# Kernel optimization log

Measured on AMD Instinct MI355X. Metric: run time of the kernel, lower is better.

The kernel has to match this reference:

```python
import jax, jax.numpy as jnp
import numpy as np

XMIN, XMAX = -16.0, 16.0
ZMIN, ZMAX = -16.0, 16.0
SOFTCLIP_L = 5.0


def ref2mem(traj, Zs, Xs):
    # traj: (B, T, 2) cam (x, z) -> mem pixel coords
    x = (traj[..., 0] - XMIN) / ((XMAX - XMIN) / Xs) - 0.5
    z = (traj[..., 1] - ZMIN) / ((ZMAX - ZMIN) / Zs) - 0.5
    return x, z


def bilinear_sample2d(pm, x, z):
    # pm: (B, C, Z, X); x, z: (B, N) float coords -> (B, C, N)
    B, C, Zs, Xs = pm.shape
    x = jnp.clip(x, 0.0, Xs - 1.0)
    z = jnp.clip(z, 0.0, Zs - 1.0)
    x0 = jnp.floor(x).astype(jnp.int32)
    z0 = jnp.floor(z).astype(jnp.int32)
    x1 = jnp.minimum(x0 + 1, Xs - 1)
    z1 = jnp.minimum(z0 + 1, Zs - 1)
    wx = x - x0.astype(x.dtype)
    wz = z - z0.astype(z.dtype)
    pm_flat = pm.reshape(B, C, Zs * Xs)

    def gather(zi, xi):
        idx = (zi * Xs + xi)[:, None, :]  # (B,1,N)
        return jnp.take_along_axis(pm_flat, jnp.broadcast_to(idx, (B, C, idx.shape[-1])), axis=2)

    v00 = gather(z0, x0); v01 = gather(z0, x1)
    v10 = gather(z1, x0); v11 = gather(z1, x1)
    wx = wx[:, None, :]; wz = wz[:, None, :]
    return (v00 * (1 - wx) * (1 - wz) + v01 * wx * (1 - wz)
            + v10 * (1 - wx) * wz + v11 * wx * wz)


def gru_cell(x, h, W_ih, W_hh, b_ih, b_hh):
    gi = x @ W_ih.T + b_ih
    gh = h @ W_hh.T + b_hh
    i_r, i_z, i_n = jnp.split(gi, 3, axis=1)
    h_r, h_z, h_n = jnp.split(gh, 3, axis=1)
    r = jax.nn.sigmoid(i_r + h_r)
    z = jax.nn.sigmoid(i_z + h_z)
    n = jnp.tanh(i_n + r * h_n)
    return (1.0 - z) * n + z * h


def expm_softclip(sig_raw):
    B = sig_raw.shape[0]
    nrm = jnp.linalg.norm(sig_raw.reshape(B, -1), axis=1)
    denom = jax.nn.logsumexp(jnp.stack([nrm / SOFTCLIP_L, jnp.ones_like(nrm)], axis=-1), axis=-1)
    return sig_raw / denom[:, None, None]


def reference(feat_map, pred_map, noise, traj_past,
              W_ih, W_hh, b_ih, b_hh, past_W, past_b,
              W1, b1, W2, b2, W3, b3):
    B, C, Zf, Xf = feat_map.shape
    Zp, Xp = pred_map.shape[2], pred_map.shape[3]
    T_futu = noise.shape[1]
    H = W_hh.shape[1]
    eye2 = jnp.eye(2, dtype=feat_map.dtype)

    # static feature: max_pool2d k=8 s=8 + past encoding
    pooled = feat_map.reshape(B, C, Zf // 8, 8, Xf // 8, 8).max(axis=(3, 5)).reshape(B, -1)
    past_enc = traj_past.reshape(B, -1) @ past_W.T + past_b
    sta_feat = jnp.concatenate([pooled, past_enc], axis=1)  # (B, 2080)

    def step(carry, noise_t):
        hx, win = carry
        xm, zm = ref2mem(win, Zp, Xp)
        feats = bilinear_sample2d(pred_map, xm, zm).reshape(B, -1)  # (B, 3)
        dyn_feat = jnp.concatenate([feats, win.reshape(B, -1)], axis=1)  # (B, 9)
        hx = gru_cell(dyn_feat, hx, W_ih, W_hh, b_ih, b_hh)
        joint = jnp.concatenate([hx, sta_feat], axis=1)  # (B, 2112)
        h1 = jax.nn.leaky_relu(joint @ W1.T + b1)
        h2 = jax.nn.leaky_relu(h1 @ W2.T + b2)
        pred = h2 @ W3.T + b3  # (B, 6)
        mu = pred[:, :2]
        sig_raw = pred[:, 2:].reshape(B, 2, 2) + 1e-8 * eye2
        sig_raw = expm_softclip(sig_raw)
        sig = jnp.einsum('bij,bkj->bik', sig_raw, sig_raw)
        xdotdot = mu + jnp.sum(sig * noise_t[:, None, :], axis=1)
        x_next = 2.0 * win[:, -1] - win[:, -2] + xdotdot  # verlet, dt=1
        win = jnp.concatenate([win[:, 1:], x_next[:, None]], axis=1)
        return (hx, win), x_next

    hx0 = jnp.zeros((B, H), dtype=feat_map.dtype)
    (_, _), traj_futu = jax.lax.scan(step, (hx0, traj_past), jnp.swapaxes(noise, 0, 1))
    return jnp.swapaxes(traj_futu, 0, 1)  # (B, T_futu, 2)


def setup_inputs():
    key = jax.random.key(0)
    ks = jax.random.split(key, 16)
    B, C, Zf, Xf = 192, 32, 64, 64
    T_futu, T_past, H = 27, 3, 32
    d = {}
    d['feat_map'] = jax.random.normal(ks[0], (B, C, Zf, Xf), jnp.float32)
    d['pred_map'] = jax.random.normal(ks[1], (B, 1, Zf, Xf), jnp.float32)
    d['noise'] = jax.random.normal(ks[2], (B, T_futu, 2), jnp.float32)
    d['traj_past'] = jax.random.normal(ks[3], (B, T_past, 2), jnp.float32) * 4.0
    s = 0.05
    d['W_ih'] = jax.random.normal(ks[4], (3 * H, 9), jnp.float32) * s
    d['W_hh'] = jax.random.normal(ks[5], (3 * H, H), jnp.float32) * s
    d['b_ih'] = jnp.zeros((3 * H,), jnp.float32)
    d['b_hh'] = jnp.zeros((3 * H,), jnp.float32)
    d['past_W'] = jax.random.normal(ks[6], (32, T_past * 2), jnp.float32) * s
    d['past_b'] = jnp.zeros((32,), jnp.float32)
    d['W1'] = jax.random.normal(ks[7], (64, 2112), jnp.float32) * 0.02
    d['b1'] = jnp.zeros((64,), jnp.float32)
    d['W2'] = jax.random.normal(ks[8], (32, 64), jnp.float32) * s
    d['b2'] = jnp.zeros((32,), jnp.float32)
    d['W3'] = jax.random.normal(ks[9], (6, 32), jnp.float32) * s
    d['b3'] = jnp.zeros((6,), jnp.float32)
    return d
```

## Files before the change

### kernel.cpp

```cpp
#include <hip/hip_runtime.h>
#include <hip/hip_bf16.h>
#include <math.h>

typedef unsigned int u32;
typedef __fp16 f16x2 __attribute__((ext_vector_type(2)));
typedef u32 u32x4 __attribute__((ext_vector_type(4)));

#define NB    192
#define NC    32
#define TFUT  27
#define BLOB_F_OFF (NB * 64)

#if __has_builtin(__builtin_amdgcn_rcpf)
#define RCPF(x) __builtin_amdgcn_rcpf(x)
#else
#define RCPF(x) (1.0f / (x))
#endif
#if __has_builtin(__builtin_amdgcn_sqrtf)
#define SQRTF(x) __builtin_amdgcn_sqrtf(x)
#else
#define SQRTF(x) sqrtf(x)
#endif
#if __has_builtin(__builtin_amdgcn_exp2f)
#define EXP2F(x) __builtin_amdgcn_exp2f(x)
#else
#define EXP2F(x) exp2f(x)
#endif
#if __has_builtin(__builtin_amdgcn_logf)
#define LOG2F(x) __builtin_amdgcn_logf(x)
#else
#define LOG2F(x) log2f(x)
#endif

__device__ __forceinline__ u32 pk16(float lo, float hi) {
    auto v = __builtin_amdgcn_cvt_pkrtz(lo, hi);
    return __builtin_bit_cast(u32, v);
}
__device__ __forceinline__ float fdot2pk(u32 a, u32 b, float c) {
#if __has_builtin(__builtin_amdgcn_fdot2)
    return __builtin_amdgcn_fdot2(__builtin_bit_cast(f16x2, a),
                                  __builtin_bit_cast(f16x2, b), c, false);
#else
    f16x2 av = __builtin_bit_cast(f16x2, a), bv = __builtin_bit_cast(f16x2, b);
    return c + (float)av[0] * (float)bv[0] + (float)av[1] * (float)bv[1];
#endif
}
__device__ __forceinline__ u32 rdl(u32 v, int lane) {
    return (u32)__builtin_amdgcn_readlane((int)v, lane);
}
__device__ __forceinline__ float rdlf(float v, int lane) {
    return __int_as_float(__builtin_amdgcn_readlane(__float_as_int(v), lane));
}
__device__ __forceinline__ float dpp_xor1(float v) {
    return __int_as_float(__builtin_amdgcn_update_dpp(
        0, __float_as_int(v), 0xB1, 0xF, 0xF, true));
}
__device__ __forceinline__ float sigmoid_f(float x) {
    return RCPF(1.0f + EXP2F(-1.4426950408889634f * x));
}
__device__ __forceinline__ float tanh_f(float x) {
    return __builtin_fmaf(2.0f, RCPF(1.0f + EXP2F(-2.8853900817779268f * x)), -1.0f);
}

__global__ __launch_bounds__(1024) void k_static(
    const float* __restrict__ feat,
    const float* __restrict__ traj_past,
    const float* __restrict__ past_W,
    const float* __restrict__ past_b,
    const float* __restrict__ W1,
    const float* __restrict__ b1,
    const float* __restrict__ W_ih,
    const float* __restrict__ W_hh,
    const float* __restrict__ b_ih,
    const float* __restrict__ b_hh,
    const float* __restrict__ W2,
    const float* __restrict__ b2,
    const float* __restrict__ W3,
    const float* __restrict__ b3,
    float* __restrict__ ws)
{
    const int b = blockIdx.x;
    const int t = threadIdx.x;

    if (b == NB) {
        if (t >= 64) return;
        const int l = t, m2 = l & 31;
        u32* blob = reinterpret_cast<u32*>(ws) + BLOB_F_OFF + (size_t)l * 128;
        #pragma unroll
        for (int k = 0; k < 9; ++k) {
            blob[k]     = __float_as_uint(W_ih[l * 9 + k]);
            blob[9 + k] = __float_as_uint(W_ih[(64 + m2) * 9 + k]);
        }
        #pragma unroll
        for (int j = 0; j < 16; ++j) {
            blob[18 + j] = pk16(W_hh[l * 32 + 2*j],          W_hh[l * 32 + 2*j + 1]);
            blob[34 + j] = pk16(W_hh[(64 + m2) * 32 + 2*j],  W_hh[(64 + m2) * 32 + 2*j + 1]);
            blob[50 + j] = pk16(W1[(size_t)l * 2112 + 2*j],  W1[(size_t)l * 2112 + 2*j + 1]);
        }
        #pragma unroll
        for (int j = 0; j < 32; ++j)
            blob[66 + j] = pk16(W2[m2 * 64 + 2*j], W2[m2 * 64 + 2*j + 1]);
        const int wr = (l < 6) ? l : 0;
        #pragma unroll
        for (int j = 0; j < 16; ++j)
            blob[98 + j] = pk16(W3[wr * 32 + 2*j], W3[wr * 32 + 2*j + 1]);
        blob[114] = __float_as_uint(b_ih[l]);
        blob[115] = __float_as_uint(b_hh[l]);
        blob[116] = __float_as_uint(b_ih[64 + m2]);
        blob[117] = __float_as_uint(b_hh[64 + m2]);
        blob[118] = __float_as_uint(b2[m2]);
        #pragma unroll
        for (int r = 0; r < 6; ++r) blob[119 + r] = __float_as_uint(b3[r]);
        blob[125] = blob[126] = blob[127] = 0u;
        return;
    }

    __shared__ __align__(16) float sta[2080];

    for (int it = 0; it < 2; ++it) {
        const int c    = it * 16 + (t >> 6);
        const int cell = t & 63;
        const int zi = cell >> 3, xi = cell & 7;
        const float* p = feat + ((size_t)b * NC + c) * 4096 + zi * 8 * 64 + xi * 8;
        float m = -3.402823466e38f;
        #pragma unroll
        for (int dz = 0; dz < 8; ++dz) {
            const float4 v0 = *reinterpret_cast<const float4*>(p + dz * 64);
            const float4 v1 = *reinterpret_cast<const float4*>(p + dz * 64 + 4);
            m = fmaxf(m, fmaxf(fmaxf(fmaxf(v0.x, v0.y), fmaxf(v0.z, v0.w)),
                               fmaxf(fmaxf(v1.x, v1.y), fmaxf(v1.z, v1.w))));
        }
        sta[c * 64 + cell] = m;
    }
    if (t < 32) {
        float acc = past_b[t];
        #pragma unroll
        for (int k = 0; k < 6; ++k) acc += past_W[t * 6 + k] * traj_past[b * 6 + k];
        sta[2048 + t] = acc;
    }
    __syncthreads();

    const int o = t >> 4, l = t & 15;
    const float* wrow = W1 + (size_t)o * 2112 + 32;
    float acc = 0.f;
    #pragma unroll 4
    for (int j = 0; j < 32; ++j) {
        const int k = j * 64 + l * 4;
        const float4 w = *reinterpret_cast<const float4*>(wrow + k);
        const float4 s = *reinterpret_cast<const float4*>(&sta[k]);
        acc += w.x * s.x + w.y * s.y + w.z * s.z + w.w * s.w;
    }
    if (l < 8) {
        const int k = 2048 + l * 4;
        const float4 w = *reinterpret_cast<const float4*>(wrow + k);
        const float4 s = *reinterpret_cast<const float4*>(&sta[k]);
        acc += w.x * s.x + w.y * s.y + w.z * s.z + w.w * s.w;
    }
    acc += __shfl_xor(acc, 1);
    acc += __shfl_xor(acc, 2);
    acc += __shfl_xor(acc, 4);
    acc += __shfl_xor(acc, 8);
    if (l == 0) ws[b * 64 + o] = b1[o] + acc;
}

__global__ __launch_bounds__(64, 1) void k_recur(
    const float* __restrict__ pred_map,
    const float* __restrict__ noise,
    const float* __restrict__ traj_past,
    const float* __restrict__ ws,
    float* __restrict__ out)
{
    __shared__ __align__(16) float pm[4096];
    __shared__ __align__(8)  float nz[56];

    const int b = blockIdx.x;
    const int l = threadIdx.x;

    {
        const float4* src = reinterpret_cast<const float4*>(pred_map + (size_t)b * 4096);
        float4* dst = reinterpret_cast<float4*>(pm);
        #pragma unroll
        for (int i = 0; i < 16; ++i) dst[l + i * 64] = src[l + i * 64];
    }
    if (l < TFUT * 2) nz[l] = noise[b * (TFUT * 2) + l];

    const u32* blob = reinterpret_cast<const u32*>(ws) + BLOB_F_OFF + (size_t)l * 128;
    u32x4 dv[32];
    #pragma unroll
    for (int j = 0; j < 32; ++j)
        dv[j] = reinterpret_cast<const u32x4*>(blob)[j];
#define DW(i) (dv[(i) >> 2][(i) & 3])
#define DF(i) __int_as_float((int)DW(i))

    const float sta1l = ws[b * 64 + l];

    float w[6];
    #pragma unroll
    for (int j = 0; j < 6; ++j) w[j] = traj_past[b * 6 + j];
    float hxloc = 0.f;
    u32 hxpk[16];
    #pragma unroll
    for (int j = 0; j < 16; ++j) hxpk[j] = 0u;
    float Adot = 0.f, Cdot = 0.f;

    __syncthreads();

    auto bsample = [&](float px, float pz) -> float {
        float x = (px + 16.0f) * 2.0f - 0.5f;
        float z = (pz + 16.0f) * 2.0f - 0.5f;
        x = fminf(fmaxf(x, 0.0f), 63.0f);
        z = fminf(fmaxf(z, 0.0f), 63.0f);
        const float xf = floorf(x), zf = floorf(z);
        const int x0 = (int)xf, z0 = (int)zf;
        const int x1 = min(x0 + 1, 63), z1 = min(z0 + 1, 63);
        const float wx = x - xf, wz = z - zf;
        const float v00 = pm[z0 * 64 + x0], v01 = pm[z0 * 64 + x1];
        const float v10 = pm[z1 * 64 + x0], v11 = pm[z1 * 64 + x1];
        return v00 * (1.f - wx) * (1.f - wz) + v01 * wx * (1.f - wz)
             + v10 * (1.f - wx) * wz        + v11 * wx * wz;
    };
    float s0 = bsample(w[0], w[1]);
    float s1 = bsample(w[2], w[3]);
    float s2 = bsample(w[4], w[5]);

    for (int ts = 0; ts < TFUT; ++ts) {
        const float2 nn = *reinterpret_cast<const float2*>(&nz[2 * ts]);

        float gi  = DF(114) + DF(3) * w[0] + DF(4) * w[1] + DF(5) * w[2]
                            + DF(6) * w[3] + DF(7) * w[4] + DF(8) * w[5];
        float gi2 = DF(116) + DF(12) * w[0] + DF(13) * w[1] + DF(14) * w[2]
                            + DF(15) * w[3] + DF(16) * w[4] + DF(17) * w[5];
        gi  += DF(0) * s0 + DF(1) * s1 + DF(2) * s2;
        gi2 += DF(9) * s0 + DF(10) * s1 + DF(11) * s2;

        const float gs   = gi + DF(115) + Adot;
        const float gh2v = DF(117) + Cdot;
        const float sg = sigmoid_f(gs);
        const float zv = __shfl_xor(sg, 32, 64);
        const float nv = tanh_f(gi2 + sg * gh2v);
        const float hnew = (1.0f - zv) * nv + zv * hxloc;
        hxloc = hnew;

        const u32 hpk = pk16(hnew, dpp_xor1(hnew));
        #pragma unroll
        for (int j = 0; j < 16; ++j) hxpk[j] = rdl(hpk, 2 * j);

        {
            float A0 = 0.f, A1 = 0.f, A2 = 0.f, A3 = 0.f;
            float C0 = 0.f, C1 = 0.f, C2 = 0.f, C3 = 0.f;
            #pragma unroll
            for (int j = 0; j < 16; j += 4) {
                A0 = fdot2pk(hxpk[j],   DW(18 + j),     A0);
                A1 = fdot2pk(hxpk[j+1], DW(18 + j + 1), A1);
                A2 = fdot2pk(hxpk[j+2], DW(18 + j + 2), A2);
                A3 = fdot2pk(hxpk[j+3], DW(18 + j + 3), A3);
                C0 = fdot2pk(hxpk[j],   DW(34 + j),     C0);
                C1 = fdot2pk(hxpk[j+1], DW(34 + j + 1), C1);
                C2 = fdot2pk(hxpk[j+2], DW(34 + j + 2), C2);
                C3 = fdot2pk(hxpk[j+3], DW(34 + j + 3), C3);
            }
            Adot = (A0 + A1) + (A2 + A3);
            Cdot = (C0 + C1) + (C2 + C3);
        }

        float D0 = 0.f, D1 = 0.f, D2 = 0.f, D3 = 0.f;
        #pragma unroll
        for (int j = 0; j < 16; j += 4) {
            D0 = fdot2pk(hxpk[j],   DW(50 + j),     D0);
            D1 = fdot2pk(hxpk[j+1], DW(50 + j + 1), D1);
            D2 = fdot2pk(hxpk[j+2], DW(50 + j + 2), D2);
            D3 = fdot2pk(hxpk[j+3], DW(50 + j + 3), D3);
        }
        const float h1a = sta1l + ((D0 + D1) + (D2 + D3));
        const float h1l = (h1a >= 0.f) ? h1a : 0.01f * h1a;

        const u32 h1p = pk16(h1l, dpp_xor1(h1l));
        u32 h1pk[32];
        #pragma unroll
        for (int j = 0; j < 32; ++j) h1pk[j] = rdl(h1p, 2 * j);

        float P0 = 0.f, P1 = 0.f, P2 = 0.f, P3 = 0.f;
        float P4 = 0.f, P5 = 0.f, P6 = 0.f, P7 = 0.f;
        #pragma unroll
        for (int j = 0; j < 32; j += 8) {
            P0 = fdot2pk(h1pk[j],   DW(66 + j),     P0);
            P1 = fdot2pk(h1pk[j+1], DW(66 + j + 1), P1);
            P2 = fdot2pk(h1pk[j+2], DW(66 + j + 2), P2);
            P3 = fdot2pk(h1pk[j+3], DW(66 + j + 3), P3);
            P4 = fdot2pk(h1pk[j+4], DW(66 + j + 4), P4);
            P5 = fdot2pk(h1pk[j+5], DW(66 + j + 5), P5);
            P6 = fdot2pk(h1pk[j+6], DW(66 + j + 6), P6);
            P7 = fdot2pk(h1pk[j+7], DW(66 + j + 7), P7);
        }
        const float h2a = DF(118) + (((P0 + P1) + (P2 + P3)) + ((P4 + P5) + (P6 + P7)));
        const float h2l = (h2a >= 0.f) ? h2a : 0.01f * h2a;

        const u32 h2p = pk16(h2l, dpp_xor1(h2l));
        u32 h2pk[16];
        #pragma unroll
        for (int j = 0; j < 16; ++j) h2pk[j] = rdl(h2p, 2 * j);

        float Q0 = 0.f, Q1 = 0.f, Q2 = 0.f, Q3 = 0.f;
        #pragma unroll
        for (int j = 0; j < 16; j += 4) {
            Q0 = fdot2pk(h2pk[j],   DW(98 + j),     Q0);
            Q1 = fdot2pk(h2pk[j+1], DW(98 + j + 1), Q1);
            Q2 = fdot2pk(h2pk[j+2], DW(98 + j + 2), Q2);
            Q3 = fdot2pk(h2pk[j+3], DW(98 + j + 3), Q3);
        }
        const float praw = (Q0 + Q1) + (Q2 + Q3);

        const float pv0 = rdlf(praw, 0) + DF(119);
        const float pv1 = rdlf(praw, 1) + DF(120);
        const float pv2 = rdlf(praw, 2) + DF(121);
        const float pv3 = rdlf(praw, 3) + DF(122);
        const float pv4 = rdlf(praw, 4) + DF(123);
        const float pv5 = rdlf(praw, 5) + DF(124);

        float s00 = pv2 + 1e-8f, s01 = pv3;
        float s10 = pv4,          s11 = pv5 + 1e-8f;
        const float nrm = SQRTF(s00 * s00 + s01 * s01 + s10 * s10 + s11 * s11);
        const float arg = nrm * 0.2f;
        const float mm  = fmaxf(arg, 1.0f);
        const float dd  = fabsf(arg - 1.0f);
        const float denom = mm + 0.6931471805599453f *
                            LOG2F(1.0f + EXP2F(-1.4426950408889634f * dd));
        const float inv = RCPF(denom);
        s00 *= inv; s01 *= inv; s10 *= inv; s11 *= inv;
        const float sig00 = s00 * s00 + s01 * s01;
        const float sig01 = s00 * s10 + s01 * s11;
        const float sig11 = s10 * s10 + s11 * s11;
        const float xd0 = pv0 + nn.x * (sig00 + sig01);
        const float xd1 = pv1 + nn.y * (sig01 + sig11);
        const float nx0 = 2.0f * w[4] - w[2] + xd0;
        const float nx1 = 2.0f * w[5] - w[3] + xd1;

        if (l == 0) {
            float2 o; o.x = nx0; o.y = nx1;
            *reinterpret_cast<float2*>(out + ((size_t)b * TFUT + ts) * 2) = o;
        }

        w[0] = w[2]; w[1] = w[3];
        w[2] = w[4]; w[3] = w[5];
        w[4] = nx0;  w[5] = nx1;
        s0 = s1; s1 = s2;
        s2 = bsample(nx0, nx1);
    }
#undef DW
#undef DF
}

extern "C" void kernel_launch(void* const* d_in, const int* in_sizes, int n_in,
                              void* d_out, int out_size, void* d_ws, size_t ws_size,
                              hipStream_t stream) {
    const float* feat      = (const float*)d_in[0];
    const float* pred_map  = (const float*)d_in[1];
    const float* noise     = (const float*)d_in[2];
    const float* traj_past = (const float*)d_in[3];
    const float* W_ih      = (const float*)d_in[4];
    const float* W_hh      = (const float*)d_in[5];
    const float* b_ih      = (const float*)d_in[6];
    const float* b_hh      = (const float*)d_in[7];
    const float* past_W    = (const float*)d_in[8];
    const float* past_b    = (const float*)d_in[9];
    const float* W1        = (const float*)d_in[10];
    const float* b1        = (const float*)d_in[11];
    const float* W2        = (const float*)d_in[12];
    const float* b2        = (const float*)d_in[13];
    const float* W3        = (const float*)d_in[14];
    const float* b3        = (const float*)d_in[15];
    float* outp = (float*)d_out;
    float* ws   = (float*)d_ws;

    k_static<<<dim3(NB + 1), dim3(1024), 0, stream>>>(
        feat, traj_past, past_W, past_b, W1, b1,
        W_ih, W_hh, b_ih, b_hh, W2, b2, W3, b3, ws);
    k_recur<<<dim3(NB), dim3(64), 0, stream>>>(pred_map, noise, traj_past, ws, outp);
}
```

Measured before the change: 47.18 us.

## Interleave two batch recurrences per wave and broadcast hidden states via LDS

The recurrent kernel now runs two batch elements in one 64-lane wavefront, launching 96 blocks instead of 192. The two independent GRU/MLP chains are interleaved stage by stage so each chain's latency can be hidden by the other's work. Hidden-state broadcasts switch from many readlane calls to fp16 writes into shared memory followed by vector reads. The gate-swap shuffle now uses v_permlane32_swap. The cost is more registers and a longer per-step instruction stream for each wave, on a kernel whose runtime is set by its serial dependency chain.

Measured after the change: 62.95 us. 1.33x slower.

```diff
diff --git a/kernel.cpp b/kernel.cpp
--- a/kernel.cpp
+++ b/kernel.cpp
@@ -9,6 +9,7 @@
 #define NB    192
 #define NC    32
 #define TFUT  27
+#define NPAIR 96
 #define BLOB_F_OFF (NB * 64)
 
 #if __has_builtin(__builtin_amdgcn_rcpf)
@@ -45,15 +46,13 @@
     return c + (float)av[0] * (float)bv[0] + (float)av[1] * (float)bv[1];
 #endif
 }
-__device__ __forceinline__ u32 rdl(u32 v, int lane) {
-    return (u32)__builtin_amdgcn_readlane((int)v, lane);
-}
 __device__ __forceinline__ float rdlf(float v, int lane) {
     return __int_as_float(__builtin_amdgcn_readlane(__float_as_int(v), lane));
 }
-__device__ __forceinline__ float dpp_xor1(float v) {
-    return __int_as_float(__builtin_amdgcn_update_dpp(
-        0, __float_as_int(v), 0xB1, 0xF, 0xF, true));
+__device__ __forceinline__ float perm32hi(float v) {
+    int x = __float_as_int(v), y = x;
+    asm volatile("v_permlane32_swap_b32 %0, %1" : "+v"(x), "+v"(y));
+    return __int_as_float(x);
 }
 __device__ __forceinline__ float sigmoid_f(float x) {
     return RCPF(1.0f + EXP2F(-1.4426950408889634f * x));
@@ -170,19 +169,23 @@
     const float* __restrict__ ws,
     float* __restrict__ out)
 {
-    __shared__ __align__(16) float pm[4096];
-    __shared__ __align__(8)  float nz[56];
-
-    const int b = blockIdx.x;
+    __shared__ __align__(16) float  pm[2][4096];
+    __shared__ __align__(16) float  nzs[2][56];
+    __shared__ __align__(16) __fp16 hxb[2][64];
+    __shared__ __align__(16) __fp16 h1b[2][64];
+    __shared__ __align__(16) __fp16 h2b[2][64];
+
     const int l = threadIdx.x;
-
-    {
-        const float4* src = reinterpret_cast<const float4*>(pred_map + (size_t)b * 4096);
-        float4* dst = reinterpret_cast<float4*>(pm);
+    const int bb[2] = { (int)blockIdx.x, (int)blockIdx.x + NPAIR };
+
+    #pragma unroll
+    for (int s = 0; s < 2; ++s) {
+        const float4* src = reinterpret_cast<const float4*>(pred_map + (size_t)bb[s] * 4096);
+        float4* dst = reinterpret_cast<float4*>(&pm[s][0]);
         #pragma unroll
         for (int i = 0; i < 16; ++i) dst[l + i * 64] = src[l + i * 64];
-    }
-    if (l < TFUT * 2) nz[l] = noise[b * (TFUT * 2) + l];
+        if (l < TFUT * 2) nzs[s][l] = noise[bb[s] * (TFUT * 2) + l];
+    }
 
     const u32* blob = reinterpret_cast<const u32*>(ws) + BLOB_F_OFF + (size_t)l * 128;
     u32x4 dv[32];
@@ -192,20 +195,19 @@
 #define DW(i) (dv[(i) >> 2][(i) & 3])
 #define DF(i) __int_as_float((int)DW(i))
 
-    const float sta1l = ws[b * 64 + l];
-
-    float w[6];
+    float sta1l[2] = { ws[bb[0] * 64 + l], ws[bb[1] * 64 + l] };
+    float w[2][6];
     #pragma unroll
-    for (int j = 0; j < 6; ++j) w[j] = traj_past[b * 6 + j];
-    float hxloc = 0.f;
-    u32 hxpk[16];
-    #pragma unroll
-    for (int j = 0; j < 16; ++j) hxpk[j] = 0u;
-    float Adot = 0.f, Cdot = 0.f;
+    for (int s = 0; s < 2; ++s)
+        #pragma unroll
+        for (int j = 0; j < 6; ++j) w[s][j] = traj_past[bb[s] * 6 + j];
+    float hxp[2]  = { 0.f, 0.f };
+    float Adot[2] = { 0.f, 0.f };
+    float Cdot[2] = { 0.f, 0.f };
 
     __syncthreads();
 
-    auto bsample = [&](float px, float pz) -> float {
+    auto bsamp = [&](int s, float px, float pz) -> float {
         float x = (px + 16.0f) * 2.0f - 0.5f;
         float z = (pz + 16.0f) * 2.0f - 0.5f;
         x = fminf(fmaxf(x, 0.0f), 63.0f);
@@ -214,138 +216,138 @@
         const int x0 = (int)xf, z0 = (int)zf;
         const int x1 = min(x0 + 1, 63), z1 = min(z0 + 1, 63);
         const float wx = x - xf, wz = z - zf;
-        const float v00 = pm[z0 * 64 + x0], v01 = pm[z0 * 64 + x1];
-        const float v10 = pm[z1 * 64 + x0], v11 = pm[z1 * 64 + x1];
+        const float v00 = pm[s][z0 * 64 + x0], v01 = pm[s][z0 * 64 + x1];
+        const float v10 = pm[s][z1 * 64 + x0], v11 = pm[s][z1 * 64 + x1];
         return v00 * (1.f - wx) * (1.f - wz) + v01 * wx * (1.f - wz)
              + v10 * (1.f - wx) * wz        + v11 * wx * wz;
     };
-    float s0 = bsample(w[0], w[1]);
-    float s1 = bsample(w[2], w[3]);
-    float s2 = bsample(w[4], w[5]);
+
+    float sm0[2], sm1[2], sm2[2];
+    #pragma unroll
+    for (int s = 0; s < 2; ++s) {
+        sm0[s] = bsamp(s, w[s][0], w[s][1]);
+        sm1[s] = bsamp(s, w[s][2], w[s][3]);
+        sm2[s] = bsamp(s, w[s][4], w[s][5]);
+    }
+
+    u32x4 hx4[2][4], h14[2][8], h24[2][4];
+
+#define GATES(S) { \
+    float gi  = DF(114) + DF(3)*w[S][0] + DF(4)*w[S][1] + DF(5)*w[S][2] \
+                        + DF(6)*w[S][3] + DF(7)*w[S][4] + DF(8)*w[S][5]; \
+    float gi2 = DF(116) + DF(12)*w[S][0] + DF(13)*w[S][1] + DF(14)*w[S][2] \
+                        + DF(15)*w[S][3] + DF(16)*w[S][4] + DF(17)*w[S][5]; \
+    gi  += DF(0)*sm0[S] + DF(1)*sm1[S] + DF(2)*sm2[S]; \
+    gi2 += DF(9)*sm0[S] + DF(10)*sm1[S] + DF(11)*sm2[S]; \
+    const float gs = gi + DF(115) + Adot[S]; \
+    const float sg = sigmoid_f(gs); \
+    const float zv = perm32hi(sg); \
+    const float nv = tanh_f(gi2 + sg * (DF(117) + Cdot[S])); \
+    const float hn = (1.0f - zv) * nv + zv * hxp[S]; \
+    hxp[S] = hn; \
+    hxb[S][l] = (__fp16)hn; \
+    const u32x4* _p = reinterpret_cast<const u32x4*>(&hxb[S][0]); \
+    _Pragma("unroll") for (int q = 0; q < 4; ++q) hx4[S][q] = _p[q]; }
+
+#define DOTS1(S) { \
+    float A0=0.f,A1=0.f,A2=0.f,A3=0.f,C0=0.f,C1=0.f,C2=0.f,C3=0.f; \
+    float D0=0.f,D1=0.f,D2=0.f,D3=0.f; \
+    _Pragma("unroll") for (int q = 0; q < 4; ++q) { \
+        const u32 p0 = hx4[S][q][0], p1 = hx4[S][q][1]; \
+        const u32 p2 = hx4[S][q][2], p3 = hx4[S][q][3]; \
+        const int j = q * 4; \
+        A0 = fdot2pk(p0, DW(18+j),   A0); A1 = fdot2pk(p1, DW(19+j), A1); \
+        A2 = fdot2pk(p2, DW(20+j),   A2); A3 = fdot2pk(p3, DW(21+j), A3); \
+        C0 = fdot2pk(p0, DW(34+j),   C0); C1 = fdot2pk(p1, DW(35+j), C1); \
+        C2 = fdot2pk(p2, DW(36+j),   C2); C3 = fdot2pk(p3, DW(37+j), C3); \
+        D0 = fdot2pk(p0, DW(50+j),   D0); D1 = fdot2pk(p1, DW(51+j), D1); \
+        D2 = fdot2pk(p2, DW(52+j),   D2); D3 = fdot2pk(p3, DW(53+j), D3); } \
+    Adot[S] = (A0 + A1) + (A2 + A3); \
+    Cdot[S] = (C0 + C1) + (C2 + C3); \
+    const float h1a = sta1l[S] + ((D0 + D1) + (D2 + D3)); \
+    const float h1l = (h1a >= 0.f) ? h1a : 0.01f * h1a; \
+    h1b[S][l] = (__fp16)h1l; \
+    const u32x4* _p = reinterpret_cast<const u32x4*>(&h1b[S][0]); \
+    _Pragma("unroll") for (int q = 0; q < 8; ++q) h14[S][q] = _p[q]; }
+
+#define DOTS2(S) { \
+    float P0=0.f,P1=0.f,P2=0.f,P3=0.f,P4=0.f,P5=0.f,P6=0.f,P7=0.f; \
+    _Pragma("unroll") for (int q = 0; q < 8; q += 2) { \
+        const int j = q * 4; \
+        P0 = fdot2pk(h14[S][q][0],   DW(66+j), P0); \
+        P1 = fdot2pk(h14[S][q][1],   DW(67+j), P1); \
+        P2 = fdot2pk(h14[S][q][2],   DW(68+j), P2); \
+        P3 = fdot2pk(h14[S][q][3],   DW(69+j), P3); \
+        P4 = fdot2pk(h14[S][q+1][0], DW(70+j), P4); \
+        P5 = fdot2pk(h14[S][q+1][1], DW(71+j), P5); \
+        P6 = fdot2pk(h14[S][q+1][2], DW(72+j), P6); \
+        P7 = fdot2pk(h14[S][q+1][3], DW(73+j), P7); } \
+    const float h2a = DF(118) + (((P0+P1)+(P2+P3)) + ((P4+P5)+(P6+P7))); \
+    const float h2l = (h2a >= 0.f) ? h2a : 0.01f * h2a; \
+    h2b[S][l] = (__fp16)h2l; \
+    const u32x4* _p = reinterpret_cast<const u32x4*>(&h2b[S][0]); \
+    _Pragma("unroll") for (int q = 0; q < 4; ++q) h24[S][q] = _p[q]; }
+
+#define TAIL(S) { \
+    float Q0=0.f,Q1=0.f,Q2=0.f,Q3=0.f; \
+    _Pragma("unroll") for (int q = 0; q < 4; ++q) { \
+        const int j = q * 4; \
+        Q0 = fdot2pk(h24[S][q][0], DW(98+j),  Q0); \
+        Q1 = fdot2pk(h24[S][q][1], DW(99+j),  Q1); \
+        Q2 = fdot2pk(h24[S][q][2], DW(100+j), Q2); \
+        Q3 = fdot2pk(h24[S][q][3], DW(101+j), Q3); } \
+    const float praw = (Q0 + Q1) + (Q2 + Q3); \
+    const float pv0 = rdlf(praw, 0) + DF(119); \
+    const float pv1 = rdlf(praw, 1) + DF(120); \
+    const float pv2 = rdlf(praw, 2) + DF(121); \
+    const float pv3 = rdlf(praw, 3) + DF(122); \
+    const float pv4 = rdlf(praw, 4) + DF(123); \
+    const float pv5 = rdlf(praw, 5) + DF(124); \
+    float s00 = pv2 + 1e-8f, s01 = pv3; \
+    float s10 = pv4,          s11 = pv5 + 1e-8f; \
+    const float nrm = SQRTF(s00*s00 + s01*s01 + s10*s10 + s11*s11); \
+    const float arg = nrm * 0.2f; \
+    const float mmx = fmaxf(arg, 1.0f); \
+    const float dd  = fabsf(arg - 1.0f); \
+    const float den = mmx + 0.6931471805599453f * \
+                      LOG2F(1.0f + EXP2F(-1.4426950408889634f * dd)); \
+    const float inv = RCPF(den); \
+    s00 *= inv; s01 *= inv; s10 *= inv; s11 *= inv; \
+    const float sig00 = s00*s00 + s01*s01; \
+    const float sig01 = s00*s10 + s01*s11; \
+    const float sig11 = s10*s10 + s11*s11; \
+    const float xd0 = pv0 + nnv[S][0] * (sig00 + sig01); \
+    const float xd1 = pv1 + nnv[S][1] * (sig01 + sig11); \
+    const float nx0 = 2.0f * w[S][4] - w[S][2] + xd0; \
+    const float nx1 = 2.0f * w[S][5] - w[S][3] + xd1; \
+    if (l == 0) { \
+        float2 o; o.x = nx0; o.y = nx1; \
+        *reinterpret_cast<float2*>(out + ((size_t)bb[S] * TFUT + ts) * 2) = o; \
+    } \
+    w[S][0] = w[S][2]; w[S][1] = w[S][3]; \
+    w[S][2] = w[S][4]; w[S][3] = w[S][5]; \
+    w[S][4] = nx0;     w[S][5] = nx1; \
+    sm0[S] = sm1[S]; sm1[S] = sm2[S]; \
+    sm2[S] = bsamp(S, nx0, nx1); }
 
     for (int ts = 0; ts < TFUT; ++ts) {
-        const float2 nn = *reinterpret_cast<const float2*>(&nz[2 * ts]);
-
-        float gi  = DF(114) + DF(3) * w[0] + DF(4) * w[1] + DF(5) * w[2]
-                            + DF(6) * w[3] + DF(7) * w[4] + DF(8) * w[5];
-        float gi2 = DF(116) + DF(12) * w[0] + DF(13) * w[1] + DF(14) * w[2]
-                            + DF(15) * w[3] + DF(16) * w[4] + DF(17) * w[5];
-        gi  += DF(0) * s0 + DF(1) * s1 + DF(2) * s2;
-        gi2 += DF(9) * s0 + DF(10) * s1 + DF(11) * s2;
-
-        const float gs   = gi + DF(115) + Adot;
-        const float gh2v = DF(117) + Cdot;
-        const float sg = sigmoid_f(gs);
-        const float zv = __shfl_xor(sg, 32, 64);
-        const float nv = tanh_f(gi2 + sg * gh2v);
-        const float hnew = (1.0f - zv) * nv + zv * hxloc;
-        hxloc = hnew;
-
-        const u32 hpk = pk16(hnew, dpp_xor1(hnew));
-        #pragma unroll
-        for (int j = 0; j < 16; ++j) hxpk[j] = rdl(hpk, 2 * j);
-
-        {
-            float A0 = 0.f, A1 = 0.f, A2 = 0.f, A3 = 0.f;
-            float C0 = 0.f, C1 = 0.f, C2 = 0.f, C3 = 0.f;
-            #pragma unroll
-            for (int j = 0; j < 16; j += 4) {
-                A0 = fdot2pk(hxpk[j],   DW(18 + j),     A0);
-                A1 = fdot2pk(hxpk[j+1], DW(18 + j + 1), A1);
-                A2 = fdot2pk(hxpk[j+2], DW(18 + j + 2), A2);
-                A3 = fdot2pk(hxpk[j+3], DW(18 + j + 3), A3);
-                C0 = fdot2pk(hxpk[j],   DW(34 + j),     C0);
-                C1 = fdot2pk(hxpk[j+1], DW(34 + j + 1), C1);
-                C2 = fdot2pk(hxpk[j+2], DW(34 + j + 2), C2);
-                C3 = fdot2pk(hxpk[j+3], DW(34 + j + 3), C3);
-            }
-            Adot = (A0 + A1) + (A2 + A3);
-            Cdot = (C0 + C1) + (C2 + C3);
-        }
-
-        float D0 = 0.f, D1 = 0.f, D2 = 0.f, D3 = 0.f;
-        #pragma unroll
-        for (int j = 0; j < 16; j += 4) {
-            D0 = fdot2pk(hxpk[j],   DW(50 + j),     D0);
-            D1 = fdot2pk(hxpk[j+1], DW(50 + j + 1), D1);
-            D2 = fdot2pk(hxpk[j+2], DW(50 + j + 2), D2);
-            D3 = fdot2pk(hxpk[j+3], DW(50 + j + 3), D3);
-        }
-        const float h1a = sta1l + ((D0 + D1) + (D2 + D3));
-        const float h1l = (h1a >= 0.f) ? h1a : 0.01f * h1a;
-
-        const u32 h1p = pk16(h1l, dpp_xor1(h1l));
-        u32 h1pk[32];
-        #pragma unroll
-        for (int j = 0; j < 32; ++j) h1pk[j] = rdl(h1p, 2 * j);
-
-        float P0 = 0.f, P1 = 0.f, P2 = 0.f, P3 = 0.f;
-        float P4 = 0.f, P5 = 0.f, P6 = 0.f, P7 = 0.f;
-        #pragma unroll
-        for (int j = 0; j < 32; j += 8) {
-            P0 = fdot2pk(h1pk[j],   DW(66 + j),     P0);
-            P1 = fdot2pk(h1pk[j+1], DW(66 + j + 1), P1);
-            P2 = fdot2pk(h1pk[j+2], DW(66 + j + 2), P2);
-            P3 = fdot2pk(h1pk[j+3], DW(66 + j + 3), P3);
-            P4 = fdot2pk(h1pk[j+4], DW(66 + j + 4), P4);
-            P5 = fdot2pk(h1pk[j+5], DW(66 + j + 5), P5);
-            P6 = fdot2pk(h1pk[j+6], DW(66 + j + 6), P6);
-            P7 = fdot2pk(h1pk[j+7], DW(66 + j + 7), P7);
-        }
-        const float h2a = DF(118) + (((P0 + P1) + (P2 + P3)) + ((P4 + P5) + (P6 + P7)));
-        const float h2l = (h2a >= 0.f) ? h2a : 0.01f * h2a;
-
-        const u32 h2p = pk16(h2l, dpp_xor1(h2l));
-        u32 h2pk[16];
-        #pragma unroll
-        for (int j = 0; j < 16; ++j) h2pk[j] = rdl(h2p, 2 * j);
-
-        float Q0 = 0.f, Q1 = 0.f, Q2 = 0.f, Q3 = 0.f;
-        #pragma unroll
-        for (int j = 0; j < 16; j += 4) {
-            Q0 = fdot2pk(h2pk[j],   DW(98 + j),     Q0);
-            Q1 = fdot2pk(h2pk[j+1], DW(98 + j + 1), Q1);
-            Q2 = fdot2pk(h2pk[j+2], DW(98 + j + 2), Q2);
-            Q3 = fdot2pk(h2pk[j+3], DW(98 + j + 3), Q3);
-        }
-        const float praw = (Q0 + Q1) + (Q2 + Q3);
-
-        const float pv0 = rdlf(praw, 0) + DF(119);
-        const float pv1 = rdlf(praw, 1) + DF(120);
-        const float pv2 = rdlf(praw, 2) + DF(121);
-        const float pv3 = rdlf(praw, 3) + DF(122);
-        const float pv4 = rdlf(praw, 4) + DF(123);
-        const float pv5 = rdlf(praw, 5) + DF(124);
-
-        float s00 = pv2 + 1e-8f, s01 = pv3;
-        float s10 = pv4,          s11 = pv5 + 1e-8f;
-        const float nrm = SQRTF(s00 * s00 + s01 * s01 + s10 * s10 + s11 * s11);
-        const float arg = nrm * 0.2f;
-        const float mm  = fmaxf(arg, 1.0f);
-        const float dd  = fabsf(arg - 1.0f);
-        const float denom = mm + 0.6931471805599453f *
-                            LOG2F(1.0f + EXP2F(-1.4426950408889634f * dd));
-        const float inv = RCPF(denom);
-        s00 *= inv; s01 *= inv; s10 *= inv; s11 *= inv;
-        const float sig00 = s00 * s00 + s01 * s01;
-        const float sig01 = s00 * s10 + s01 * s11;
-        const float sig11 = s10 * s10 + s11 * s11;
-        const float xd0 = pv0 + nn.x * (sig00 + sig01);
-        const float xd1 = pv1 + nn.y * (sig01 + sig11);
-        const float nx0 = 2.0f * w[4] - w[2] + xd0;
-        const float nx1 = 2.0f * w[5] - w[3] + xd1;
-
-        if (l == 0) {
-            float2 o; o.x = nx0; o.y = nx1;
-            *reinterpret_cast<float2*>(out + ((size_t)b * TFUT + ts) * 2) = o;
-        }
-
-        w[0] = w[2]; w[1] = w[3];
-        w[2] = w[4]; w[3] = w[5];
-        w[4] = nx0;  w[5] = nx1;
-        s0 = s1; s1 = s2;
-        s2 = bsample(nx0, nx1);
-    }
+        float nnv[2][2];
+        nnv[0][0] = nzs[0][2*ts]; nnv[0][1] = nzs[0][2*ts + 1];
+        nnv[1][0] = nzs[1][2*ts]; nnv[1][1] = nzs[1][2*ts + 1];
+
+        GATES(0)
+        GATES(1)
+        DOTS1(0)
+        DOTS1(1)
+        DOTS2(0)
+        DOTS2(1)
+        TAIL(0)
+        TAIL(1)
+    }
+#undef GATES
+#undef DOTS1
+#undef DOTS2
+#undef TAIL
 #undef DW
 #undef DF
 }
@@ -375,5 +377,5 @@
     k_static<<<dim3(NB + 1), dim3(1024), 0, stream>>>(
         feat, traj_past, past_W, past_b, W1, b1,
         W_ih, W_hh, b_ih, b_hh, W2, b2, W3, b3, ws);
-    k_recur<<<dim3(NB), dim3(64), 0, stream>>>(pred_map, noise, traj_past, ws, outp);
-}
+    k_recur<<<dim3(NPAIR), dim3(64), 0, stream>>>(pred_map, noise, traj_past, ws, outp);
+}
```

## Overlap GRU hidden matvecs with bilinear LDS loads and use permlane32 swap

Applied to the files above, without the earlier changes.

Reorders the recurrent loop so the MLP head runs first. The next step's hidden-state dot products (Adot/Cdot) are then computed while the bilinear-sample LDS loads are in flight, hiding LDS latency on the serial critical path. It also replaces the cross-half shuffle with v_permlane32_swap, keeps the noise in a register read via readlane instead of LDS, and computes sigma from the unnormalised products scaled by inv squared. The inline asm is specific to gfx950 and the algebraic rescaling slightly changes rounding.

Measured after the change: 45.91 us. 2.7% less time.

```diff
diff --git a/kernel.cpp b/kernel.cpp
--- a/kernel.cpp
+++ b/kernel.cpp
@@ -54,6 +54,11 @@
 __device__ __forceinline__ float dpp_xor1(float v) {
     return __int_as_float(__builtin_amdgcn_update_dpp(
         0, __float_as_int(v), 0xB1, 0xF, 0xF, true));
+}
+__device__ __forceinline__ float perm32hi(float v) {
+    int x = __float_as_int(v), y = x;
+    asm volatile("v_permlane32_swap_b32 %0, %1" : "+v"(x), "+v"(y));
+    return __int_as_float(x);
 }
 __device__ __forceinline__ float sigmoid_f(float x) {
     return RCPF(1.0f + EXP2F(-1.4426950408889634f * x));
@@ -171,7 +176,6 @@
     float* __restrict__ out)
 {
     __shared__ __align__(16) float pm[4096];
-    __shared__ __align__(8)  float nz[56];
 
     const int b = blockIdx.x;
     const int l = threadIdx.x;
@@ -182,7 +186,7 @@
         #pragma unroll
         for (int i = 0; i < 16; ++i) dst[l + i * 64] = src[l + i * 64];
     }
-    if (l < TFUT * 2) nz[l] = noise[b * (TFUT * 2) + l];
+    const float nzreg = (l < TFUT * 2) ? noise[b * (TFUT * 2) + l] : 0.f;
 
     const u32* blob = reinterpret_cast<const u32*>(ws) + BLOB_F_OFF + (size_t)l * 128;
     u32x4 dv[32];
@@ -197,7 +201,7 @@
     float w[6];
     #pragma unroll
     for (int j = 0; j < 6; ++j) w[j] = traj_past[b * 6 + j];
-    float hxloc = 0.f;
+    float hxp = 0.f;
     u32 hxpk[16];
     #pragma unroll
     for (int j = 0; j < 16; ++j) hxpk[j] = 0u;
@@ -205,7 +209,7 @@
 
     __syncthreads();
 
-    auto bsample = [&](float px, float pz) -> float {
+    auto bsamp = [&](float px, float pz) -> float {
         float x = (px + 16.0f) * 2.0f - 0.5f;
         float z = (pz + 16.0f) * 2.0f - 0.5f;
         x = fminf(fmaxf(x, 0.0f), 63.0f);
@@ -219,31 +223,127 @@
         return v00 * (1.f - wx) * (1.f - wz) + v01 * wx * (1.f - wz)
              + v10 * (1.f - wx) * wz        + v11 * wx * wz;
     };
-    float s0 = bsample(w[0], w[1]);
-    float s1 = bsample(w[2], w[3]);
-    float s2 = bsample(w[4], w[5]);
+    float sm0 = bsamp(w[0], w[1]);
+    float sm1 = bsamp(w[2], w[3]);
+    float sm2 = bsamp(w[4], w[5]);
 
     for (int ts = 0; ts < TFUT; ++ts) {
-        const float2 nn = *reinterpret_cast<const float2*>(&nz[2 * ts]);
-
         float gi  = DF(114) + DF(3) * w[0] + DF(4) * w[1] + DF(5) * w[2]
                             + DF(6) * w[3] + DF(7) * w[4] + DF(8) * w[5];
         float gi2 = DF(116) + DF(12) * w[0] + DF(13) * w[1] + DF(14) * w[2]
                             + DF(15) * w[3] + DF(16) * w[4] + DF(17) * w[5];
-        gi  += DF(0) * s0 + DF(1) * s1 + DF(2) * s2;
-        gi2 += DF(9) * s0 + DF(10) * s1 + DF(11) * s2;
-
-        const float gs   = gi + DF(115) + Adot;
-        const float gh2v = DF(117) + Cdot;
+        gi  += DF(0) * sm0 + DF(1) * sm1 + DF(2) * sm2;
+        gi2 += DF(9) * sm0 + DF(10) * sm1 + DF(11) * sm2;
+
+        const float gs = gi + DF(115) + Adot;
         const float sg = sigmoid_f(gs);
-        const float zv = __shfl_xor(sg, 32, 64);
-        const float nv = tanh_f(gi2 + sg * gh2v);
-        const float hnew = (1.0f - zv) * nv + zv * hxloc;
-        hxloc = hnew;
-
-        const u32 hpk = pk16(hnew, dpp_xor1(hnew));
+        const float zv = perm32hi(sg);
+        const float nv = tanh_f(gi2 + sg * (DF(117) + Cdot));
+        const float hn = (1.0f - zv) * nv + zv * hxp;
+        hxp = hn;
+
+        const u32 hpk = pk16(hn, dpp_xor1(hn));
         #pragma unroll
         for (int j = 0; j < 16; ++j) hxpk[j] = rdl(hpk, 2 * j);
+
+        float D0 = 0.f, D1 = 0.f, D2 = 0.f, D3 = 0.f;
+        #pragma unroll
+        for (int j = 0; j < 16; j += 4) {
+            D0 = fdot2pk(hxpk[j],   DW(50 + j),     D0);
+            D1 = fdot2pk(hxpk[j+1], DW(50 + j + 1), D1);
+            D2 = fdot2pk(hxpk[j+2], DW(50 + j + 2), D2);
+            D3 = fdot2pk(hxpk[j+3], DW(50 + j + 3), D3);
+        }
+        const float h1a = sta1l + ((D0 + D1) + (D2 + D3));
+        const float h1l = (h1a >= 0.f) ? h1a : 0.01f * h1a;
+
+        const u32 h1p = pk16(h1l, dpp_xor1(h1l));
+        u32 h1pk[32];
+        #pragma unroll
+        for (int j = 0; j < 32; ++j) h1pk[j] = rdl(h1p, 2 * j);
+
+        float P0 = 0.f, P1 = 0.f, P2 = 0.f, P3 = 0.f;
+        float P4 = 0.f, P5 = 0.f, P6 = 0.f, P7 = 0.f;
+        #pragma unroll
+        for (int j = 0; j < 32; j += 8) {
+            P0 = fdot2pk(h1pk[j],   DW(66 + j),     P0);
+            P1 = fdot2pk(h1pk[j+1], DW(66 + j + 1), P1);
+            P2 = fdot2pk(h1pk[j+2], DW(66 + j + 2), P2);
+            P3 = fdot2pk(h1pk[j+3], DW(66 + j + 3), P3);
+            P4 = fdot2pk(h1pk[j+4], DW(66 + j + 4), P4);
+            P5 = fdot2pk(h1pk[j+5], DW(66 + j + 5), P5);
+            P6 = fdot2pk(h1pk[j+6], DW(66 + j + 6), P6);
+            P7 = fdot2pk(h1pk[j+7], DW(66 + j + 7), P7);
+        }
+        const float h2a = DF(118) + (((P0 + P1) + (P2 + P3)) + ((P4 + P5) + (P6 + P7)));
+        const float h2l = (h2a >= 0.f) ? h2a : 0.01f * h2a;
+
+        const u32 h2p = pk16(h2l, dpp_xor1(h2l));
+        u32 h2pk[16];
+        #pragma unroll
+        for (int j = 0; j < 16; ++j) h2pk[j] = rdl(h2p, 2 * j);
+
+        float Q0 = 0.f, Q1 = 0.f, Q2 = 0.f, Q3 = 0.f;
+        #pragma unroll
+        for (int j = 0; j < 16; j += 4) {
+            Q0 = fdot2pk(h2pk[j],   DW(98 + j),     Q0);
+            Q1 = fdot2pk(h2pk[j+1], DW(98 + j + 1), Q1);
+            Q2 = fdot2pk(h2pk[j+2], DW(98 + j + 2), Q2);
+            Q3 = fdot2pk(h2pk[j+3], DW(98 + j + 3), Q3);
+        }
+        const float praw = (Q0 + Q1) + (Q2 + Q3);
+
+        const float pv0 = rdlf(praw, 0) + DF(119);
+        const float pv1 = rdlf(praw, 1) + DF(120);
+        const float pv2 = rdlf(praw, 2) + DF(121);
+        const float pv3 = rdlf(praw, 3) + DF(122);
+        const float pv4 = rdlf(praw, 4) + DF(123);
+        const float pv5 = rdlf(praw, 5) + DF(124);
+
+        const float s00 = pv2 + 1e-8f, s01 = pv3;
+        const float s10 = pv4,          s11 = pv5 + 1e-8f;
+        const float p00 = s00 * s00 + s01 * s01;
+        const float p01 = s00 * s10 + s01 * s11;
+        const float p11 = s10 * s10 + s11 * s11;
+        const float nrm = SQRTF(p00 + p11);
+        const float arg = nrm * 0.2f;
+        const float mmx = fmaxf(arg, 1.0f);
+        const float dd  = fabsf(arg - 1.0f);
+        const float den = mmx + 0.6931471805599453f *
+                          LOG2F(1.0f + EXP2F(-1.4426950408889634f * dd));
+        const float inv  = RCPF(den);
+        const float inv2 = inv * inv;
+
+        const float nnx = rdlf(nzreg, 2 * ts);
+        const float nny = rdlf(nzreg, 2 * ts + 1);
+        const float xd0 = pv0 + nnx * ((p00 + p01) * inv2);
+        const float xd1 = pv1 + nny * ((p01 + p11) * inv2);
+        const float nx0 = 2.0f * w[4] - w[2] + xd0;
+        const float nx1 = 2.0f * w[5] - w[3] + xd1;
+
+        if (l == 0) {
+            float2 o; o.x = nx0; o.y = nx1;
+            *reinterpret_cast<float2*>(out + ((size_t)b * TFUT + ts) * 2) = o;
+        }
+
+        w[0] = w[2]; w[1] = w[3];
+        w[2] = w[4]; w[3] = w[5];
+        w[4] = nx0;  w[5] = nx1;
+        sm0 = sm1; sm1 = sm2;
+
+        float v00, v01, v10, v11, wxs, wzs;
+        {
+            float x = (nx0 + 16.0f) * 2.0f - 0.5f;
+            float z = (nx1 + 16.0f) * 2.0f - 0.5f;
+            x = fminf(fmaxf(x, 0.0f), 63.0f);
+            z = fminf(fmaxf(z, 0.0f), 63.0f);
+            const float xf = floorf(x), zf = floorf(z);
+            const int x0 = (int)xf, z0 = (int)zf;
+            const int x1 = min(x0 + 1, 63), z1 = min(z0 + 1, 63);
+            wxs = x - xf; wzs = z - zf;
+            v00 = pm[z0 * 64 + x0]; v01 = pm[z0 * 64 + x1];
+            v10 = pm[z1 * 64 + x0]; v11 = pm[z1 * 64 + x1];
+        }
 
         {
             float A0 = 0.f, A1 = 0.f, A2 = 0.f, A3 = 0.f;
@@ -263,88 +363,8 @@
             Cdot = (C0 + C1) + (C2 + C3);
         }
 
-        float D0 = 0.f, D1 = 0.f, D2 = 0.f, D3 = 0.f;
-        #pragma unroll
-        for (int j = 0; j < 16; j += 4) {
-            D0 = fdot2pk(hxpk[j],   DW(50 + j),     D0);
-            D1 = fdot2pk(hxpk[j+1], DW(50 + j + 1), D1);
-            D2 = fdot2pk(hxpk[j+2], DW(50 + j + 2), D2);
-            D3 = fdot2pk(hxpk[j+3], DW(50 + j + 3), D3);
-        }
-        const float h1a = sta1l + ((D0 + D1) + (D2 + D3));
-        const float h1l = (h1a >= 0.f) ? h1a : 0.01f * h1a;
-
-        const u32 h1p = pk16(h1l, dpp_xor1(h1l));
-        u32 h1pk[32];
-        #pragma unroll
-        for (int j = 0; j < 32; ++j) h1pk[j] = rdl(h1p, 2 * j);
-
-        float P0 = 0.f, P1 = 0.f, P2 = 0.f, P3 = 0.f;
-        float P4 = 0.f, P5 = 0.f, P6 = 0.f, P7 = 0.f;
-        #pragma unroll
-        for (int j = 0; j < 32; j += 8) {
-            P0 = fdot2pk(h1pk[j],   DW(66 + j),     P0);
-            P1 = fdot2pk(h1pk[j+1], DW(66 + j + 1), P1);
-            P2 = fdot2pk(h1pk[j+2], DW(66 + j + 2), P2);
-            P3 = fdot2pk(h1pk[j+3], DW(66 + j + 3), P3);
-            P4 = fdot2pk(h1pk[j+4], DW(66 + j + 4), P4);
-            P5 = fdot2pk(h1pk[j+5], DW(66 + j + 5), P5);
-            P6 = fdot2pk(h1pk[j+6], DW(66 + j + 6), P6);
-            P7 = fdot2pk(h1pk[j+7], DW(66 + j + 7), P7);
-        }
-        const float h2a = DF(118) + (((P0 + P1) + (P2 + P3)) + ((P4 + P5) + (P6 + P7)));
-        const float h2l = (h2a >= 0.f) ? h2a : 0.01f * h2a;
-
-        const u32 h2p = pk16(h2l, dpp_xor1(h2l));
-        u32 h2pk[16];
-        #pragma unroll
-        for (int j = 0; j < 16; ++j) h2pk[j] = rdl(h2p, 2 * j);
-
-        float Q0 = 0.f, Q1 = 0.f, Q2 = 0.f, Q3 = 0.f;
-        #pragma unroll
-        for (int j = 0; j < 16; j += 4) {
-            Q0 = fdot2pk(h2pk[j],   DW(98 + j),     Q0);
-            Q1 = fdot2pk(h2pk[j+1], DW(98 + j + 1), Q1);
-            Q2 = fdot2pk(h2pk[j+2], DW(98 + j + 2), Q2);
-            Q3 = fdot2pk(h2pk[j+3], DW(98 + j + 3), Q3);
-        }
-        const float praw = (Q0 + Q1) + (Q2 + Q3);
-
-        const float pv0 = rdlf(praw, 0) + DF(119);
-        const float pv1 = rdlf(praw, 1) + DF(120);
-        const float pv2 = rdlf(praw, 2) + DF(121);
-        const float pv3 = rdlf(praw, 3) + DF(122);
-        const float pv4 = rdlf(praw, 4) + DF(123);
-        const float pv5 = rdlf(praw, 5) + DF(124);
-
-        float s00 = pv2 + 1e-8f, s01 = pv3;
-        float s10 = pv4,          s11 = pv5 + 1e-8f;
-        const float nrm = SQRTF(s00 * s00 + s01 * s01 + s10 * s10 + s11 * s11);
-        const float arg = nrm * 0.2f;
-        const float mm  = fmaxf(arg, 1.0f);
-        const float dd  = fabsf(arg - 1.0f);
-        const float denom = mm + 0.6931471805599453f *
-                            LOG2F(1.0f + EXP2F(-1.4426950408889634f * dd));
-        const float inv = RCPF(denom);
-        s00 *= inv; s01 *= inv; s10 *= inv; s11 *= inv;
-        const float sig00 = s00 * s00 + s01 * s01;
-        const float sig01 = s00 * s10 + s01 * s11;
-        const float sig11 = s10 * s10 + s11 * s11;
-        const float xd0 = pv0 + nn.x * (sig00 + sig01);
-        const float xd1 = pv1 + nn.y * (sig01 + sig11);
-        const float nx0 = 2.0f * w[4] - w[2] + xd0;
-        const float nx1 = 2.0f * w[5] - w[3] + xd1;
-
-        if (l == 0) {
-            float2 o; o.x = nx0; o.y = nx1;
-            *reinterpret_cast<float2*>(out + ((size_t)b * TFUT + ts) * 2) = o;
-        }
-
-        w[0] = w[2]; w[1] = w[3];
-        w[2] = w[4]; w[3] = w[5];
-        w[4] = nx0;  w[5] = nx1;
-        s0 = s1; s1 = s2;
-        s2 = bsample(nx0, nx1);
+        sm2 = v00 * (1.f - wxs) * (1.f - wzs) + v01 * wxs * (1.f - wzs)
+            + v10 * (1.f - wxs) * wzs        + v11 * wxs * wzs;
     }
 #undef DW
 #undef DF
```
